# Performance work log

Measured on AMD Instinct MI355X. Metric: run time of the kernel, lower is better.

Reference implementation:

```python
import jax, jax.numpy as jnp
import numpy as np

D_MODEL = 1024
N_HEADS = 16
D_K = D_MODEL // N_HEADS


def setup_inputs() -> dict:
    key = jax.random.key(0)
    ks = jax.random.split(key, 12)
    B, S, D, H = 2, 2048, D_MODEL, N_HEADS
    s = 1.0 / np.sqrt(D)
    inp = {
        "x": jax.random.normal(ks[0], (B, S, D), jnp.float32),
        "Wq": jax.random.normal(ks[1], (D, D), jnp.float32) * s,
        "bq": jnp.zeros((D,), jnp.float32),
        "Wk": jax.random.normal(ks[2], (D, D), jnp.float32) * s,
        "bk": jnp.zeros((D,), jnp.float32),
        "Wv": jax.random.normal(ks[3], (D, D), jnp.float32) * s,
        "bv": jnp.zeros((D,), jnp.float32),
        "Wo": jax.random.normal(ks[4], (D, D), jnp.float32) * s,
        "bo": jnp.zeros((D,), jnp.float32),
        "Wp": jax.random.normal(ks[5], (D, H), jnp.float32) * s,
        "bp": jnp.zeros((H,), jnp.float32),
        "alpha": jax.random.normal(ks[6], (H,), jnp.float32) * 0.1,
    }
    return inp


def reference(x, Wq, bq, Wk, bk, Wv, bv, Wo, bo, Wp, bp, alpha):
    B, S, D = x.shape
    H, dk = N_HEADS, D_K
    scale = dk ** -0.5
    # projections -> (B, H, S, dk)
    Q = (x @ Wq + bq).reshape(B, S, H, dk).transpose(0, 2, 1, 3)
    K = (x @ Wk + bk).reshape(B, S, H, dk).transpose(0, 2, 1, 3)
    V = (x @ Wv + bv).reshape(B, S, H, dk).transpose(0, 2, 1, 3)
    scores = jnp.einsum("bhid,bhjd->bhij", Q, K) * scale  # (B,H,S,S)
    # phase derived from x: (B,S,H) -> (B,H,S)
    phase = (x @ Wp + bp).transpose(0, 2, 1)
    # coherence(i,j) = cos(phi_i - phi_j), per batch/head
    coherence = jnp.cos(phase[:, :, :, None] - phase[:, :, None, :])
    scores = scores + alpha[None, :, None, None] * coherence
    attn = jax.nn.softmax(scores, axis=-1)
    out = jnp.einsum("bhij,bhjd->bhid", attn, V)  # (B,H,S,dk)
    out = out.transpose(0, 2, 1, 3).reshape(B, S, D)
    return out @ Wo + bo
```

## Files before the change

kernel.cpp:

```cpp
#include <hip/hip_runtime.h>
#include <math.h>


#define S_LEN 2048
#define NHEADS 16

typedef __attribute__((ext_vector_type(8))) short short8;
typedef __attribute__((ext_vector_type(4))) float floatx4;
typedef __attribute__((ext_vector_type(2))) float float2v;
typedef __attribute__((ext_vector_type(4))) unsigned int uintx4;

__device__ inline unsigned short f2bf(float f) {
    union { float f; unsigned int i; } v; v.f = f;
    unsigned int u = v.i;
    return (unsigned short)((u + 0x7fffu + ((u >> 16) & 1u)) >> 16);
}
__device__ inline unsigned int pack2_bf16(float hi, float lo) {
    union { float f; unsigned int u; } a, b; a.f = hi; b.f = lo;
    return __builtin_amdgcn_perm(a.u, b.u, 0x07060302u);
}
__device__ inline void async_copy16(const unsigned short* src, unsigned short* dst_lds) {
    __builtin_amdgcn_global_load_lds(
        (const __attribute__((address_space(1))) unsigned int*)(src),
        (__attribute__((address_space(3))) unsigned int*)(dst_lds), 16, 0, 0);
}
__device__ inline void async_copy4(const float* src, float* dst_lds) {
    __builtin_amdgcn_global_load_lds(
        (const __attribute__((address_space(1))) unsigned int*)(src),
        (__attribute__((address_space(3))) unsigned int*)(dst_lds), 4, 0, 0);
}

__global__ __launch_bounds__(256) void prep_kernel(
    const float* __restrict__ x, const float* __restrict__ Wp,
    const float* __restrict__ bp,
    const float* __restrict__ w0, const float* __restrict__ w1,
    const float* __restrict__ w2, const float* __restrict__ w3,
    unsigned short* __restrict__ d0, unsigned short* __restrict__ d1,
    unsigned short* __restrict__ d2, unsigned short* __restrict__ d3,
    float* __restrict__ cosP, float* __restrict__ sinP,
    unsigned short* __restrict__ xb) {
    __shared__ __align__(16) unsigned short shmem[64 * 72];
    int t = threadIdx.x;
    if (blockIdx.x < 4096) {
        float* fb = reinterpret_cast<float*>(shmem);
        float* xs = fb;
        float4* red4 = reinterpret_cast<float4*>(fb + 1024);
        int bid = blockIdx.x;
        int b = bid >> 11, s = bid & 2047;
        const float* xr = x + (size_t)bid * 1024;
        float4 xv = *reinterpret_cast<const float4*>(&xr[t * 4]);
        {
            uint2 o;
            o.x = (unsigned int)f2bf(xv.x) | ((unsigned int)f2bf(xv.y) << 16);
            o.y = (unsigned int)f2bf(xv.z) | ((unsigned int)f2bf(xv.w) << 16);
            *reinterpret_cast<uint2*>(&xb[(size_t)bid * 1024 + t * 4]) = o;
        }
        *reinterpret_cast<float4*>(&xs[t * 4]) = xv;
        __syncthreads();
        float f0 = 0.f, f1 = 0.f, f2 = 0.f, f3 = 0.f;
        int krow = t >> 2;
        const float4* wp4 = reinterpret_cast<const float4*>(Wp);
#pragma unroll
        for (int i = 0; i < 16; i++) {
            float4 wv = wp4[i * 256 + t];
            float xk = xs[i * 64 + krow];
            f0 += xk * wv.x; f1 += xk * wv.y; f2 += xk * wv.z; f3 += xk * wv.w;
        }
        red4[t] = make_float4(f0, f1, f2, f3);
        __syncthreads();
        if (t < 16) {
            int b2 = t >> 2, comp = t & 3;
            const float* rf = fb + 1024;
            float sum = bp[t];
#pragma unroll
            for (int j = 0; j < 64; j++) sum += rf[(4 * j + b2) * 4 + comp];
            float sv, cv;
            __sincosf(sum, &sv, &cv);
            size_t o = ((size_t)b * NHEADS + t) * S_LEN + s;
            cosP[o] = cv; sinP[o] = sv;
        }
    } else {
        unsigned short (*tile)[72] = reinterpret_cast<unsigned short (*)[72]>(shmem);
        int bid = blockIdx.x - 4096;
        int mat = bid >> 8;
        int tl  = bid & 255;
        int tr = tl >> 4, tc = tl & 15;
        const float* src    = (mat == 0) ? w0 : (mat == 1) ? w1 : (mat == 2) ? w2 : w3;
        unsigned short* dst = (mat == 0) ? d0 : (mat == 1) ? d1 : (mat == 2) ? d2 : d3;
        int col = t & 63, rbase = (t >> 6) * 16;
#pragma unroll
        for (int i = 0; i < 16; i++) {
            int row = rbase + i;
            tile[row][col] = f2bf(src[(size_t)(tr * 64 + row) * 1024 + tc * 64 + col]);
        }
        __syncthreads();
#pragma unroll
        for (int i = 0; i < 16; i++) {
            int row = rbase + i;
            dst[(size_t)(tc * 64 + row) * 1024 + tr * 64 + col] = tile[col][row];
        }
    }
}

template <int MT>
__global__ __launch_bounds__(256) void gemm_bt(
    const unsigned short* __restrict__ A, const unsigned short* __restrict__ BT,
    int N, int mode,
    const float* __restrict__ b0, const float* __restrict__ b1,
    const float* __restrict__ b2,
    unsigned short* __restrict__ o0, unsigned short* __restrict__ o1,
    unsigned short* __restrict__ o2, float* __restrict__ of) {
    __shared__ __align__(16) unsigned short As[MT * 32];
    __shared__ __align__(16) unsigned short Bs[128 * 32];
    const int K = 1024;
    const int MI = MT / 32;
    int t = threadIdx.x;
    int mBase = blockIdx.x * MT;
    int nBase = blockIdx.y * 128;
    int w = t >> 6, lane = t & 63, l15 = lane & 15, quad = lane >> 4;
    int wm = (w & 1) * (MT / 2), wn = (w >> 1) * 64;
    floatx4 acc[MI][4];
#pragma unroll
    for (int i = 0; i < MI; i++)
#pragma unroll
        for (int j = 0; j < 4; j++) acc[i][j] = (floatx4){0.f, 0.f, 0.f, 0.f};

    int arow = t >> 2, aseg = (t & 3) * 8;
    for (int k0 = 0; k0 < K; k0 += 32) {
        __syncthreads();
#pragma unroll
        for (int i = 0; i < MT / 64; i++)
            async_copy16(&A[(size_t)(mBase + i * 64 + arow) * K + k0 + aseg],
                         &As[(i * 64 + arow) * 32 + aseg]);
#pragma unroll
        for (int i = 0; i < 2; i++)
            async_copy16(&BT[(size_t)(nBase + i * 64 + arow) * K + k0 + aseg],
                         &Bs[(i * 64 + arow) * 32 + aseg]);
        __syncthreads();
        short8 af[MI], bfr[4];
#pragma unroll
        for (int mi = 0; mi < MI; mi++)
            af[mi] = *reinterpret_cast<const short8*>(&As[(wm + mi * 16 + l15) * 32 + quad * 8]);
#pragma unroll
        for (int ni = 0; ni < 4; ni++)
            bfr[ni] = *reinterpret_cast<const short8*>(&Bs[(wn + ni * 16 + l15) * 32 + quad * 8]);
#pragma unroll
        for (int mi = 0; mi < MI; mi++)
#pragma unroll
            for (int ni = 0; ni < 4; ni++)
                acc[mi][ni] = __builtin_amdgcn_mfma_f32_16x16x32_bf16(af[mi], bfr[ni], acc[mi][ni], 0, 0, 0);
    }

#pragma unroll
    for (int mi = 0; mi < MI; mi++) {
        int rowB = mBase + wm + mi * 16 + quad * 4;
#pragma unroll
        for (int ni = 0; ni < 4; ni++) {
            int col = nBase + wn + ni * 16 + l15;
            if (mode == 0) {
                float bias = b0[col];
#pragma unroll
                for (int r = 0; r < 4; r++) {
                    of[(size_t)(rowB + r) * N + col] = acc[mi][ni][r] + bias;
                }
            } else {
                int mat = col >> 10, nn = col & 1023;
                int h = nn >> 6, d = nn & 63;
                int b = rowB >> 11, sidx = rowB & 2047;
                if (mat == 2) {
                    float bv = b2[nn];
                    int jj = sidx & 63;
                    int a2 = jj >> 5, c2 = (jj >> 4) & 1, bb = jj & 15;
                    size_t rowOff = ((size_t)((b * NHEADS + h) * 64 + d)) * S_LEN +
                                    (sidx & ~63) + a2 * 32 + c2;
#pragma unroll
                    for (int r = 0; r < 4; r++)
                        o2[rowOff + 2 * (bb + r)] = f2bf(acc[mi][ni][r] + bv);
                } else {
                    const float* bias  = (mat == 0) ? b0 : b1;
                    unsigned short* op = (mat == 0) ? o0 : o1;
                    float bv = bias[nn];
                    float scl = (mat == 0) ? 0.18033688f : 1.0f;
#pragma unroll
                    for (int r = 0; r < 4; r++) {
                        float cv = (acc[mi][ni][r] + bv) * scl;
                        op[(((size_t)b * NHEADS + h) * S_LEN + (sidx + r)) * 64 + d] = f2bf(cv);
                    }
                }
            }
        }
    }
}

__global__ __launch_bounds__(1024) void attn_kernel(
    const unsigned short* __restrict__ Qg, const unsigned short* __restrict__ Kg,
    const unsigned short* __restrict__ VTg,
    const float* __restrict__ cosP, const float* __restrict__ sinP,
    const float* __restrict__ alpha, unsigned short* __restrict__ ctx) {
    __shared__ __align__(16) unsigned short KsB[2][64 * 64];
    __shared__ __align__(16) unsigned short VtB[2][64 * 64];
    __shared__ __align__(16) float csB[2][128];
    __shared__ __align__(16) unsigned short Plb[16][16 * 72];

    int x = blockIdx.x;
    int bh = (x & 7) * 4 + (x >> 6);
    int qt = (x >> 3) & 7;
    int t = threadIdx.x, w = t >> 6, lane = t & 63, l15 = lane & 15, quad = lane >> 4;
    int m0 = qt * 256 + w * 16;
    size_t base = (size_t)bh * (S_LEN * 64);
    size_t phBase = (size_t)bh * S_LEN;
    const float L2E = 1.44269504f;

    int th = t & 511;
    int sj = th >> 3, sg = th & 7;
    int srot = ((sg - (sj & 7)) & 7) * 8;
    bool stK = (t < 512);

    short8 qf[2];
#pragma unroll
    for (int c = 0; c < 2; c++)
        qf[c] = *reinterpret_cast<const short8*>(
            &Qg[base + (size_t)(m0 + l15) * 64 + c * 32 + quad * 8]);

    float alph = alpha[bh & 15] * L2E;
    float2v ci2[2], si2[2];
#pragma unroll
    for (int hh = 0; hh < 2; hh++) {
        size_t o = phBase + m0 + quad * 4 + hh * 2;
        ci2[hh] = (float2v){alph * cosP[o], alph * cosP[o + 1]};
        si2[hh] = (float2v){alph * sinP[o], alph * sinP[o + 1]};
    }

    {
        if (stK) async_copy16(&Kg[base + (size_t)sj * 64 + srot], &KsB[0][th * 8]);
        else     async_copy16(&VTg[base + (size_t)sj * S_LEN + srot], &VtB[0][th * 8]);
        if (w == 4)      async_copy4(&cosP[phBase + lane], &csB[0][lane]);
        else if (w == 5) async_copy4(&sinP[phBase + lane], &csB[0][64 + lane]);
    }

    floatx4 oacc[4], lacc;
#pragma unroll
    for (int tt = 0; tt < 4; tt++) oacc[tt] = (floatx4){0.f, 0.f, 0.f, 0.f};
    lacc = (floatx4){0.f, 0.f, 0.f, 0.f};
    const short8 ones8 = {(short)0x3F80, (short)0x3F80, (short)0x3F80, (short)0x3F80,
                          (short)0x3F80, (short)0x3F80, (short)0x3F80, (short)0x3F80};

    int rot = l15 & 7;
    int cb0 = 16 * ((quad + rot) & 7);
    int cb1 = 16 * ((quad + 4 + rot) & 7);

    for (int kt = 0; kt < 32; kt++) {
        int p = kt & 1;
        __syncthreads();
        if (kt < 31) {
            int kn = kt + 1, pn = p ^ 1;
            if (stK) async_copy16(&Kg[base + (size_t)(kn * 64 + sj) * 64 + srot], &KsB[pn][th * 8]);
            else     async_copy16(&VTg[base + (size_t)sj * S_LEN + kn * 64 + srot], &VtB[pn][th * 8]);
            if (w == 4)      async_copy4(&cosP[phBase + kn * 64 + lane], &csB[pn][lane]);
            else if (w == 5) async_copy4(&sinP[phBase + kn * 64 + lane], &csB[pn][64 + lane]);
        }

        floatx4 st[4];
#pragma unroll
        for (int jt = 0; jt < 4; jt++) {
            const char* kr = (const char*)&KsB[p][(jt * 16 + l15) * 64];
            short8 kf0 = *reinterpret_cast<const short8*>(kr + cb0);
            short8 kf1 = *reinterpret_cast<const short8*>(kr + cb1);
            floatx4 s = (floatx4){0.f, 0.f, 0.f, 0.f};
            s = __builtin_amdgcn_mfma_f32_16x16x32_bf16(qf[0], kf0, s, 0, 0, 0);
            s = __builtin_amdgcn_mfma_f32_16x16x32_bf16(qf[1], kf1, s, 0, 0, 0);
            st[jt] = s;
        }

        float cjv[4], sjv[4];
#pragma unroll
        for (int jt = 0; jt < 4; jt++) {
            cjv[jt] = csB[p][jt * 16 + l15];
            sjv[jt] = csB[p][64 + jt * 16 + l15];
        }

        unsigned int* pl = reinterpret_cast<unsigned int*>(&Plb[w][0]);
#pragma unroll
        for (int rp = 0; rp < 2; rp++) {
            float2v a0, a1, a2, a3;
            {
                float2v s0 = (float2v){st[0][rp * 2], st[0][rp * 2 + 1]};
                float2v s1 = (float2v){st[1][rp * 2], st[1][rp * 2 + 1]};
                float2v s2 = (float2v){st[2][rp * 2], st[2][rp * 2 + 1]};
                float2v s3 = (float2v){st[3][rp * 2], st[3][rp * 2 + 1]};
                a0 = si2[rp] * sjv[0] + (ci2[rp] * cjv[0] + s0);
                a1 = si2[rp] * sjv[1] + (ci2[rp] * cjv[1] + s1);
                a2 = si2[rp] * sjv[2] + (ci2[rp] * cjv[2] + s2);
                a3 = si2[rp] * sjv[3] + (ci2[rp] * cjv[3] + s3);
            }
            int row = quad * 4 + rp * 2;
            pl[row * 36 + l15]      = pack2_bf16(__builtin_amdgcn_exp2f(a1.x),
                                                 __builtin_amdgcn_exp2f(a0.x));
            pl[row * 36 + 16 + l15] = pack2_bf16(__builtin_amdgcn_exp2f(a3.x),
                                                 __builtin_amdgcn_exp2f(a2.x));
            pl[(row + 1) * 36 + l15]      = pack2_bf16(__builtin_amdgcn_exp2f(a1.y),
                                                       __builtin_amdgcn_exp2f(a0.y));
            pl[(row + 1) * 36 + 16 + l15] = pack2_bf16(__builtin_amdgcn_exp2f(a3.y),
                                                       __builtin_amdgcn_exp2f(a2.y));
        }

        short8 pf[2];
#pragma unroll
        for (int c = 0; c < 2; c++)
            pf[c] = *reinterpret_cast<const short8*>(
                &Plb[w][l15 * 72 + c * 32 + quad * 8]);

#pragma unroll
        for (int c = 0; c < 2; c++) {
            int cb = c ? cb1 : cb0;
#pragma unroll
            for (int tt = 0; tt < 4; tt++) {
                const char* vr = (const char*)&VtB[p][(tt * 16 + l15) * 64];
                short8 vf = *reinterpret_cast<const short8*>(vr + cb);
                oacc[tt] = __builtin_amdgcn_mfma_f32_16x16x32_bf16(pf[c], vf, oacc[tt], 0, 0, 0);
            }
            lacc = __builtin_amdgcn_mfma_f32_16x16x32_bf16(pf[c], ones8, lacc, 0, 0, 0);
        }
    }

    int b = bh >> 4, h = bh & 15;
    float inv[4];
#pragma unroll
    for (int r = 0; r < 4; r++) inv[r] = 1.0f / lacc[r];
#pragma unroll
    for (int tt = 0; tt < 4; tt++)
#pragma unroll
        for (int r = 0; r < 4; r++) {
            int srow = m0 + quad * 4 + r;
            ctx[((size_t)(b * S_LEN + srow)) * 1024 + h * 64 + tt * 16 + l15] =
                f2bf(oacc[tt][r] * inv[r]);
        }
}

extern "C" void kernel_launch(void* const* d_in, const int* in_sizes, int n_in,
                              void* d_out, int out_size, void* d_ws, size_t ws_size,
                              hipStream_t stream) {
    const float* x     = (const float*)d_in[0];
    const float* Wq    = (const float*)d_in[1];
    const float* bq    = (const float*)d_in[2];
    const float* Wk    = (const float*)d_in[3];
    const float* bk    = (const float*)d_in[4];
    const float* Wv    = (const float*)d_in[5];
    const float* bv    = (const float*)d_in[6];
    const float* Wo    = (const float*)d_in[7];
    const float* bo    = (const float*)d_in[8];
    const float* Wp    = (const float*)d_in[9];
    const float* bp    = (const float*)d_in[10];
    const float* alpha = (const float*)d_in[11];
    float* out = (float*)d_out;

    const size_t MB = 1048576;
    char* ws = (char*)d_ws;
    unsigned short* WT   = (unsigned short*)(ws);
    unsigned short* WoT  = (unsigned short*)(ws + 6 * MB);
    unsigned short* xb   = (unsigned short*)(ws + 8 * MB);
    unsigned short* ctx  = (unsigned short*)(ws + 8 * MB);
    unsigned short* Qw   = (unsigned short*)(ws + 16 * MB);
    unsigned short* Kw   = (unsigned short*)(ws + 24 * MB);
    unsigned short* VTg  = (unsigned short*)(ws + 32 * MB);
    float* cosP          = (float*)(ws + 40 * MB);
    float* sinP          = (float*)(ws + 40 * MB + 262144);

    prep_kernel<<<dim3(5120), dim3(256), 0, stream>>>(
        x, Wp, bp, Wq, Wk, Wv, Wo,
        WT, WT + 1048576, WT + 2097152, WoT, cosP, sinP, xb);
    gemm_bt<128><<<dim3(32, 24), dim3(256), 0, stream>>>(
        xb, WT, 3072, 1, bq, bk, bv, Qw, Kw, VTg, (float*)nullptr);
    attn_kernel<<<dim3(256), dim3(1024), 0, stream>>>(
        Qw, Kw, VTg, cosP, sinP, alpha, ctx);
    gemm_bt<64><<<dim3(64, 8), dim3(256), 0, stream>>>(
        ctx, WoT, 1024, 0, bo, bo, bo,
        (unsigned short*)nullptr, (unsigned short*)nullptr,
        (unsigned short*)nullptr, out);
}
```

Measured before the change: 214.5 us.

## Permute V-transposed key layout for 8-byte P stores and load phases directly

The V-transposed output of the projection GEMM is written with a new key permutation inside each 64-key tile, so each lane can pack four bf16 probabilities into one 8-byte LDS store instead of two 4-byte stores per row. The cos/sin phase values for key tiles are now read straight from global memory (cached) each iteration instead of being staged through double-buffered LDS with async copies. This cuts LDS store instructions and LDS traffic, but adds global-load latency inside the inner loop and depends on the key permutation in V matching the new P column order.

```diff
diff --git a/kernel.cpp b/kernel.cpp
--- a/kernel.cpp
+++ b/kernel.cpp
@@ -23,11 +23,6 @@
     __builtin_amdgcn_global_load_lds(
         (const __attribute__((address_space(1))) unsigned int*)(src),
         (__attribute__((address_space(3))) unsigned int*)(dst_lds), 16, 0, 0);
-}
-__device__ inline void async_copy4(const float* src, float* dst_lds) {
-    __builtin_amdgcn_global_load_lds(
-        (const __attribute__((address_space(1))) unsigned int*)(src),
-        (__attribute__((address_space(3))) unsigned int*)(dst_lds), 4, 0, 0);
 }
 
 __global__ __launch_bounds__(256) void prep_kernel(
@@ -170,12 +165,14 @@
                 if (mat == 2) {
                     float bv = b2[nn];
                     int jj = sidx & 63;
-                    int a2 = jj >> 5, c2 = (jj >> 4) & 1, bb = jj & 15;
                     size_t rowOff = ((size_t)((b * NHEADS + h) * 64 + d)) * S_LEN +
-                                    (sidx & ~63) + a2 * 32 + c2;
-#pragma unroll
-                    for (int r = 0; r < 4; r++)
-                        o2[rowOff + 2 * (bb + r)] = f2bf(acc[mi][ni][r] + bv);
+                                    (sidx & ~63);
+#pragma unroll
+                    for (int r = 0; r < 4; r++) {
+                        int j2 = jj + r;
+                        int u = 4 * (j2 & 15) + (j2 >> 4);
+                        o2[rowOff + u] = f2bf(acc[mi][ni][r] + bv);
+                    }
                 } else {
                     const float* bias  = (mat == 0) ? b0 : b1;
                     unsigned short* op = (mat == 0) ? o0 : o1;
@@ -199,7 +196,6 @@
     const float* __restrict__ alpha, unsigned short* __restrict__ ctx) {
     __shared__ __align__(16) unsigned short KsB[2][64 * 64];
     __shared__ __align__(16) unsigned short VtB[2][64 * 64];
-    __shared__ __align__(16) float csB[2][128];
     __shared__ __align__(16) unsigned short Plb[16][16 * 72];
 
     int x = blockIdx.x;
@@ -234,8 +230,6 @@
     {
         if (stK) async_copy16(&Kg[base + (size_t)sj * 64 + srot], &KsB[0][th * 8]);
         else     async_copy16(&VTg[base + (size_t)sj * S_LEN + srot], &VtB[0][th * 8]);
-        if (w == 4)      async_copy4(&cosP[phBase + lane], &csB[0][lane]);
-        else if (w == 5) async_copy4(&sinP[phBase + lane], &csB[0][64 + lane]);
     }
 
     floatx4 oacc[4], lacc;
@@ -256,8 +250,17 @@
             int kn = kt + 1, pn = p ^ 1;
             if (stK) async_copy16(&Kg[base + (size_t)(kn * 64 + sj) * 64 + srot], &KsB[pn][th * 8]);
             else     async_copy16(&VTg[base + (size_t)sj * S_LEN + kn * 64 + srot], &VtB[pn][th * 8]);
-            if (w == 4)      async_copy4(&cosP[phBase + kn * 64 + lane], &csB[pn][lane]);
-            else if (w == 5) async_copy4(&sinP[phBase + kn * 64 + lane], &csB[pn][64 + lane]);
+        }
+
+        float cjv[4], sjv[4];
+        {
+            const float* cpb = &cosP[phBase + kt * 64];
+            const float* spb = &sinP[phBase + kt * 64];
+#pragma unroll
+            for (int jt = 0; jt < 4; jt++) {
+                cjv[jt] = cpb[jt * 16 + l15];
+                sjv[jt] = spb[jt * 16 + l15];
+            }
         }
 
         floatx4 st[4];
@@ -272,14 +275,7 @@
             st[jt] = s;
         }
 
-        float cjv[4], sjv[4];
-#pragma unroll
-        for (int jt = 0; jt < 4; jt++) {
-            cjv[jt] = csB[p][jt * 16 + l15];
-            sjv[jt] = csB[p][64 + jt * 16 + l15];
-        }
-
-        unsigned int* pl = reinterpret_cast<unsigned int*>(&Plb[w][0]);
+        uint2* pl2 = reinterpret_cast<uint2*>(&Plb[w][0]);
 #pragma unroll
         for (int rp = 0; rp < 2; rp++) {
             float2v a0, a1, a2, a3;
@@ -294,14 +290,18 @@
                 a3 = si2[rp] * sjv[3] + (ci2[rp] * cjv[3] + s3);
             }
             int row = quad * 4 + rp * 2;
-            pl[row * 36 + l15]      = pack2_bf16(__builtin_amdgcn_exp2f(a1.x),
-                                                 __builtin_amdgcn_exp2f(a0.x));
-            pl[row * 36 + 16 + l15] = pack2_bf16(__builtin_amdgcn_exp2f(a3.x),
-                                                 __builtin_amdgcn_exp2f(a2.x));
-            pl[(row + 1) * 36 + l15]      = pack2_bf16(__builtin_amdgcn_exp2f(a1.y),
-                                                       __builtin_amdgcn_exp2f(a0.y));
-            pl[(row + 1) * 36 + 16 + l15] = pack2_bf16(__builtin_amdgcn_exp2f(a3.y),
-                                                       __builtin_amdgcn_exp2f(a2.y));
+            {
+                uint2 o;
+                o.x = pack2_bf16(__builtin_amdgcn_exp2f(a1.x), __builtin_amdgcn_exp2f(a0.x));
+                o.y = pack2_bf16(__builtin_amdgcn_exp2f(a3.x), __builtin_amdgcn_exp2f(a2.x));
+                pl2[row * 18 + l15] = o;
+            }
+            {
+                uint2 o;
+                o.x = pack2_bf16(__builtin_amdgcn_exp2f(a1.y), __builtin_amdgcn_exp2f(a0.y));
+                o.y = pack2_bf16(__builtin_amdgcn_exp2f(a3.y), __builtin_amdgcn_exp2f(a2.y));
+                pl2[(row + 1) * 18 + l15] = o;
+            }
         }
 
         short8 pf[2];
```

New measurement: 218.4 us. About the same (+1.8%).
